# Kernel optimization log

Measured on AMD Instinct MI355X. Metric: run time of the kernel, lower is better.

Reference implementation:

```python
import jax, jax.numpy as jnp
import numpy as np

N_NODES = 100000
N_EDGES = 1600000
D = 128


def setup_inputs() -> dict:
    key = jax.random.key(0)
    ks = jax.random.split(key, 10)
    features = jax.random.normal(ks[0], (N_NODES, D), dtype=jnp.float32)
    edge_index = jax.random.randint(ks[1], (2, N_EDGES), 0, N_NODES, dtype=jnp.int64)
    edge_weight = jax.random.uniform(ks[2], (N_EDGES,), dtype=jnp.float32)
    scale = 1.0 / np.sqrt(D)
    W1 = jax.random.normal(ks[3], (D, D), dtype=jnp.float32) * scale
    b1 = jnp.zeros((D,), dtype=jnp.float32)
    a1 = jnp.full((D,), 0.25, dtype=jnp.float32)  # PReLU init
    W2 = jax.random.normal(ks[4], (D, D), dtype=jnp.float32) * scale
    b2 = jnp.zeros((D,), dtype=jnp.float32)
    a2 = jnp.full((D,), 0.25, dtype=jnp.float32)
    return {"features": features, "edge_index": edge_index, "edge_weight": edge_weight,
            "W1": W1, "b1": b1, "a1": a1, "W2": W2, "b2": b2, "a2": a2}


def _gcn_norm(edge_index, edge_weight, n_nodes):
    # PyG GCNConv default: add self-loops (weight 1), symmetric normalization.
    src, dst = edge_index[0], edge_index[1]
    loop = jnp.arange(n_nodes, dtype=src.dtype)
    src = jnp.concatenate([src, loop])
    dst = jnp.concatenate([dst, loop])
    w = jnp.concatenate([edge_weight, jnp.ones((n_nodes,), edge_weight.dtype)])
    deg = jax.ops.segment_sum(w, dst, num_segments=n_nodes)  # in-degree (target)
    dis = jnp.where(deg > 0, jax.lax.rsqrt(deg), 0.0)
    norm = dis[src] * w * dis[dst]  # [E + N]
    return src, dst, norm


def _gcn_layer(x, W, b, src, dst, norm, n_nodes):
    h = x @ W                                 # [N, D] dense GEMM first (PyG order)
    msg = h[src] * norm[:, None]              # gather + scale, [E+N, D]
    out = jax.ops.segment_sum(msg, dst, num_segments=n_nodes)
    return out + b


def _prelu(x, a):
    return jnp.where(x >= 0, x, a * x)


def reference(features, edge_index, edge_weight, W1, b1, a1, W2, b2, a2):
    n = features.shape[0]
    src, dst, norm = _gcn_norm(edge_index, edge_weight, n)
    # dropout is identity in eval mode
    x = _prelu(_gcn_layer(features, W1, b1, src, dst, norm, n), a1)
    x = _prelu(_gcn_layer(x, W2, b2, src, dst, norm, n), a2)
    return x
```

## Files before the change

kernel.cpp:

```cpp
#include <hip/hip_runtime.h>
#include <cstdint>

#define NN 100000
#define NE 1600000
#define DD 128
#define NB 250
#define BSZ 400

typedef unsigned int uint;
typedef unsigned short ushort;

typedef __attribute__((ext_vector_type(8))) short short8;
typedef __attribute__((ext_vector_type(4))) float floatx4;

__device__ inline uint f2bf(float f) {
    uint u = __float_as_uint(f);
    return (u + 0x7fffu + ((u >> 16) & 1u)) >> 16;
}


__global__ __launch_bounds__(256) void zero_bc(uint* __restrict__ bc) {
    if (threadIdx.x < NB) bc[threadIdx.x] = 0u;
}

__global__ __launch_bounds__(256) void bucket_hist(const int* __restrict__ dst,
                                                   uint* __restrict__ bc) {
    __shared__ uint h[NB];
    int tid = threadIdx.x;
    if (tid < NB) h[tid] = 0u;
    __syncthreads();
    int e0 = blockIdx.x * 8192 + tid;
#pragma unroll
    for (int k = 0; k < 32; ++k) {
        int e = e0 + 256 * k;
        if (e < NE) atomicAdd(&h[(uint)dst[e] / BSZ], 1u);
    }
    __syncthreads();
    if (tid < NB && h[tid]) atomicAdd(&bc[tid], h[tid]);
}

__global__ __launch_bounds__(256) void bucket_prefix(const uint* __restrict__ bc,
                                                     uint* __restrict__ bbase,
                                                     uint* __restrict__ bcur) {
    int lane = threadIdx.x;
    if (lane < 64) {
        uint v[4], s = 0;
#pragma unroll
        for (int k = 0; k < 4; ++k) {
            int i = lane * 4 + k;
            v[k] = (i < NB) ? bc[i] : 0u;
            s += v[k];
        }
        uint inc = s;
#pragma unroll
        for (int d = 1; d < 64; d <<= 1) {
            uint t = __shfl_up(inc, (unsigned)d, 64);
            if (lane >= d) inc += t;
        }
        uint run = inc - s;
#pragma unroll
        for (int k = 0; k < 4; ++k) {
            int i = lane * 4 + k;
            if (i < NB) { bbase[i] = run; bcur[i] = run; run += v[k]; }
        }
        if (lane == 63) bbase[NB] = run;
    }
}

__global__ __launch_bounds__(256) void bucket_append(const int* __restrict__ src,
                                                     const int* __restrict__ dst,
                                                     const float* __restrict__ w,
                                                     uint* __restrict__ bcur,
                                                     int2* __restrict__ etmp) {
    __shared__ uint h[NB];
    __shared__ uint res[NB];
    int tid = threadIdx.x;
    if (tid < NB) h[tid] = 0u;
    __syncthreads();
    int e0 = blockIdx.x * 4096 + tid;
    uint rank[16], bkt[16];
#pragma unroll
    for (int k = 0; k < 16; ++k) {
        int e = e0 + 256 * k;
        if (e < NE) {
            uint b = (uint)dst[e] / BSZ;
            bkt[k] = b;
            rank[k] = atomicAdd(&h[b], 1u);
        } else bkt[k] = 0xffffffffu;
    }
    __syncthreads();
    if (tid < NB) res[tid] = h[tid] ? atomicAdd(&bcur[tid], h[tid]) : 0u;
    __syncthreads();
#pragma unroll
    for (int k = 0; k < 16; ++k) {
        if (bkt[k] != 0xffffffffu) {
            int e = e0 + 256 * k;
            uint dl = (uint)dst[e] - bkt[k] * BSZ;
            uint wq = (uint)(w[e] * 8388608.0f);
            if (wq > 8388607u) wq = 8388607u;
            etmp[res[bkt[k]] + rank[k]] = make_int2(src[e], (int)((dl << 23) | wq));
        }
    }
}

__global__ __launch_bounds__(256) void bucket_build(const int2* __restrict__ etmp,
                                                    const uint* __restrict__ bbase,
                                                    float* __restrict__ dis,
                                                    int* __restrict__ hist_g,
                                                    int* __restrict__ rowstart,
                                                    int2* __restrict__ edges) {
    __shared__ float wdeg[BSZ];
    __shared__ uint  cnt[BSZ];
    __shared__ uint  cur[BSZ];
    __shared__ float disl[BSZ];
    int tid = threadIdx.x;
    int b = blockIdx.x;
    int n0 = b * BSZ;
    for (int i = tid; i < BSZ; i += 256) { wdeg[i] = 0.f; cnt[i] = 0u; }
    __syncthreads();
    uint base = bbase[b], end = bbase[b + 1];
    for (uint i = base + tid; i < end; i += 256) {
        uint y = (uint)etmp[i].y;
        uint dl = y >> 23;
        float wv = (float)(y & 0x7fffffu) * (1.0f / 8388608.0f);
        atomicAdd(&wdeg[dl], wv);
        atomicAdd(&cnt[dl], 1u);
    }
    __syncthreads();
    if (tid < 64) {
        uint v[7], s = 0;
#pragma unroll
        for (int k = 0; k < 7; ++k) {
            int i = tid * 7 + k;
            v[k] = (i < BSZ) ? cnt[i] : 0u;
            s += v[k];
        }
        uint inc = s;
#pragma unroll
        for (int d = 1; d < 64; d <<= 1) {
            uint t = __shfl_up(inc, (unsigned)d, 64);
            if (tid >= d) inc += t;
        }
        uint run = inc - s;
#pragma unroll
        for (int k = 0; k < 7; ++k) {
            int i = tid * 7 + k;
            if (i < BSZ) { cur[i] = run; run += v[k]; }
        }
    }
    __syncthreads();
    for (int i = tid; i < BSZ; i += 256) {
        float ds = rsqrtf(1.0f + wdeg[i]);
        disl[i] = ds;
        dis[n0 + i] = ds;
        hist_g[n0 + i] = (int)cnt[i];
        rowstart[n0 + i] = (int)(base + cur[i]);
    }
    __syncthreads();
    for (uint i = base + tid; i < end; i += 256) {
        int2 e = etmp[i];
        uint y = (uint)e.y;
        uint dl = y >> 23;
        float wv = (float)(y & 0x7fffffu) * (1.0f / 8388608.0f);
        uint p = atomicAdd(&cur[dl], 1u);
        float nrm = wv * disl[dl];
        edges[base + p] = make_int2(e.x, __float_as_int(nrm));
    }
}

#define WTS 136
__global__ __launch_bounds__(256) void gemm_mfma(const float* __restrict__ X,
                                                 const float* __restrict__ W,
                                                 const float* __restrict__ dis,
                                                 ushort* __restrict__ HB, int nrows) {
    __shared__ ushort Wt[DD * WTS];
    int tid = threadIdx.x;
#pragma unroll
    for (int it = 0; it < 16; ++it) {
        int flat = (tid + it * 256) * 4;
        int k = flat >> 7, n = flat & 127;
        float4 wv = *(const float4*)&W[flat];
        Wt[(n + 0) * WTS + k] = (ushort)f2bf(wv.x);
        Wt[(n + 1) * WTS + k] = (ushort)f2bf(wv.y);
        Wt[(n + 2) * WTS + k] = (ushort)f2bf(wv.z);
        Wt[(n + 3) * WTS + k] = (ushort)f2bf(wv.w);
    }
    __syncthreads();

    int wave = tid >> 6, lane = tid & 63;
    int q = lane >> 4, l16 = lane & 15;
    int row0 = blockIdx.x * 64 + wave * 16;

    int arow = row0 + l16;
    if (arow >= nrows) arow = nrows - 1;
    const float* xr = X + (size_t)arow * DD + q * 8;
    short8 afr[4];
#pragma unroll
    for (int ks = 0; ks < 4; ++ks) {
        float4 f0 = *(const float4*)(xr + ks * 32);
        float4 f1 = *(const float4*)(xr + ks * 32 + 4);
        uint4 u;
        u.x = f2bf(f0.x) | (f2bf(f0.y) << 16);
        u.y = f2bf(f0.z) | (f2bf(f0.w) << 16);
        u.z = f2bf(f1.x) | (f2bf(f1.y) << 16);
        u.w = f2bf(f1.z) | (f2bf(f1.w) << 16);
        afr[ks] = __builtin_bit_cast(short8, u);
    }

    floatx4 acc[8];
#pragma unroll
    for (int ct = 0; ct < 8; ++ct) acc[ct] = (floatx4)(0.0f);

#pragma unroll
    for (int ct = 0; ct < 8; ++ct) {
        const ushort* wp = &Wt[(ct * 16 + l16) * WTS + q * 8];
#pragma unroll
        for (int ks = 0; ks < 4; ++ks) {
            short8 bfr = *(const short8*)(wp + ks * 32);
            acc[ct] = __builtin_amdgcn_mfma_f32_16x16x32_bf16(afr[ks], bfr, acc[ct], 0, 0, 0);
        }
    }

#pragma unroll
    for (int reg = 0; reg < 4; ++reg) {
        int r = row0 + q * 4 + reg;
        if (r < nrows) {
            float ds = dis[r];
            ushort* orow = HB + (size_t)r * DD + l16;
#pragma unroll
            for (int ct = 0; ct < 8; ++ct)
                orow[ct * 16] = (ushort)f2bf(acc[ct][reg] * ds);
        }
    }
}

__device__ inline float4 bf4(uint2 u) {
    float4 f;
    f.x = __uint_as_float(u.x << 16);
    f.y = __uint_as_float(u.x & 0xffff0000u);
    f.z = __uint_as_float(u.y << 16);
    f.w = __uint_as_float(u.y & 0xffff0000u);
    return f;
}

__global__ __launch_bounds__(256) void gather_finalize(const ushort* __restrict__ hb,
                                                       const int2* __restrict__ edges,
                                                       const int* __restrict__ rowstart,
                                                       const int* __restrict__ hist,
                                                       const float* __restrict__ dis,
                                                       const float* __restrict__ b,
                                                       const float* __restrict__ a,
                                                       float* __restrict__ xout) {
    int tid = threadIdx.x;
    int lane = tid & 31;
    int node = blockIdx.x * 8 + (tid >> 5);

    int start = rowstart[node];
    int cnt = hist[node];
    float ds = dis[node];

    const uint2* hrow = (const uint2*)(hb + (size_t)node * DD) + lane;
    float4 self = bf4(*hrow);
    float4 acc0, acc1;
    acc0.x = self.x * ds; acc0.y = self.y * ds;
    acc0.z = self.z * ds; acc0.w = self.w * ds;
    acc1 = make_float4(0.f, 0.f, 0.f, 0.f);

    int j = 0;
    for (; j + 4 <= cnt; j += 4) {
        int2 e0 = edges[start + j];
        int2 e1 = edges[start + j + 1];
        int2 e2 = edges[start + j + 2];
        int2 e3 = edges[start + j + 3];
        uint2 u0 = *((const uint2*)(hb + (size_t)e0.x * DD) + lane);
        uint2 u1 = *((const uint2*)(hb + (size_t)e1.x * DD) + lane);
        uint2 u2 = *((const uint2*)(hb + (size_t)e2.x * DD) + lane);
        uint2 u3 = *((const uint2*)(hb + (size_t)e3.x * DD) + lane);
        float n0 = __int_as_float(e0.y), n1 = __int_as_float(e1.y);
        float n2 = __int_as_float(e2.y), n3 = __int_as_float(e3.y);
        float4 v0 = bf4(u0), v1 = bf4(u1), v2 = bf4(u2), v3 = bf4(u3);
        acc0.x += v0.x * n0; acc0.y += v0.y * n0; acc0.z += v0.z * n0; acc0.w += v0.w * n0;
        acc1.x += v1.x * n1; acc1.y += v1.y * n1; acc1.z += v1.z * n1; acc1.w += v1.w * n1;
        acc0.x += v2.x * n2; acc0.y += v2.y * n2; acc0.z += v2.z * n2; acc0.w += v2.w * n2;
        acc1.x += v3.x * n3; acc1.y += v3.y * n3; acc1.z += v3.z * n3; acc1.w += v3.w * n3;
    }
    for (; j < cnt; ++j) {
        int2 e = edges[start + j];
        uint2 u = *((const uint2*)(hb + (size_t)e.x * DD) + lane);
        float n = __int_as_float(e.y);
        float4 v = bf4(u);
        acc0.x += v.x * n; acc0.y += v.y * n; acc0.z += v.z * n; acc0.w += v.w * n;
    }

    float4 bb = ((const float4*)b)[lane];
    float4 aa = ((const float4*)a)[lane];
    float4 r;
    r.x = acc0.x + acc1.x + bb.x;
    r.y = acc0.y + acc1.y + bb.y;
    r.z = acc0.z + acc1.z + bb.z;
    r.w = acc0.w + acc1.w + bb.w;
    r.x = r.x >= 0.f ? r.x : aa.x * r.x;
    r.y = r.y >= 0.f ? r.y : aa.y * r.y;
    r.z = r.z >= 0.f ? r.z : aa.z * r.z;
    r.w = r.w >= 0.f ? r.w : aa.w * r.w;
    ((float4*)xout)[(size_t)node * 32 + lane] = r;
}

extern "C" void kernel_launch(void* const* d_in, const int* in_sizes, int n_in,
                              void* d_out, int out_size, void* d_ws, size_t ws_size,
                              hipStream_t stream) {
    const float* feat = (const float*)d_in[0];
    const int*   ei   = (const int*)d_in[1];
    const float* ew   = (const float*)d_in[2];
    const float* W1   = (const float*)d_in[3];
    const float* b1   = (const float*)d_in[4];
    const float* a1   = (const float*)d_in[5];
    const float* W2   = (const float*)d_in[6];
    const float* b2   = (const float*)d_in[7];
    const float* a2   = (const float*)d_in[8];
    float* out = (float*)d_out;

    const int* srcp = ei;
    const int* dstp = ei + NE;

    char* wsb = (char*)d_ws;
    size_t off = 0;
    uint* bc     = (uint*)(wsb + off); off += 4096;
    uint* bbase  = (uint*)(wsb + off); off += 4096;
    uint* bcur   = (uint*)(wsb + off); off += 4096;
    float* dis   = (float*)(wsb + off); off += 4ull * NN;
    int* hist    = (int*)(wsb + off); off += 4ull * NN;
    int* rowstart= (int*)(wsb + off); off += 4ull * NN;
    int2* etmp   = (int2*)(wsb + off); off += 8ull * NE;
    int2* edges  = (int2*)(wsb + off); off += 8ull * NE;
    ushort* hb   = (ushort*)(wsb + off); off += 2ull * NN * DD;
    float* x1    = out;

    zero_bc<<<1, 256, 0, stream>>>(bc);
    bucket_hist<<<(NE + 8191) / 8192, 256, 0, stream>>>(dstp, bc);
    bucket_prefix<<<1, 256, 0, stream>>>(bc, bbase, bcur);
    bucket_append<<<(NE + 4095) / 4096, 256, 0, stream>>>(srcp, dstp, ew, bcur, etmp);
    bucket_build<<<NB, 256, 0, stream>>>(etmp, bbase, dis, hist, rowstart, edges);

    const int gemm_blocks = (NN + 63) / 64;
    const int gath_blocks = NN / 8;

    gemm_mfma<<<gemm_blocks, 256, 0, stream>>>(feat, W1, dis, hb, NN);
    gather_finalize<<<gath_blocks, 256, 0, stream>>>(hb, edges, rowstart, hist, dis, b1, a1, x1);
    gemm_mfma<<<gemm_blocks, 256, 0, stream>>>(x1, W2, dis, hb, NN);
    gather_finalize<<<gath_blocks, 256, 0, stream>>>(hb, edges, rowstart, hist, dis, b2, a2, out);
}
```

Before: 375.3 us.

## Store layer-1 output as bf16, grid-stride GEMM, wider gather unroll, packed degree atomics

Layer-1 gather now writes its activations in bf16 to a new workspace buffer, and the second GEMM reads them directly without converting from fp32. This halves that intermediate traffic at the cost of rounding the stored activations to bf16. The GEMM becomes a grid-stride loop over 64-row tiles with half as many blocks, so each block's W-to-LDS transpose serves two tiles. The gather unrolls 8 edges per iteration with four accumulators to keep more loads in flight. bucket_build also packs the edge count and fixed-point weight sum into a single 64-bit LDS atomic instead of two atomics.

```diff
diff --git a/kernel.cpp b/kernel.cpp
--- a/kernel.cpp
+++ b/kernel.cpp
@@ -9,6 +9,7 @@
 
 typedef unsigned int uint;
 typedef unsigned short ushort;
+typedef unsigned long long u64;
 
 typedef __attribute__((ext_vector_type(8))) short short8;
 typedef __attribute__((ext_vector_type(4))) float floatx4;
@@ -109,22 +110,19 @@
                                                     int* __restrict__ hist_g,
                                                     int* __restrict__ rowstart,
                                                     int2* __restrict__ edges) {
-    __shared__ float wdeg[BSZ];
-    __shared__ uint  cnt[BSZ];
+    __shared__ u64   wc[BSZ];
     __shared__ uint  cur[BSZ];
     __shared__ float disl[BSZ];
     int tid = threadIdx.x;
     int b = blockIdx.x;
     int n0 = b * BSZ;
-    for (int i = tid; i < BSZ; i += 256) { wdeg[i] = 0.f; cnt[i] = 0u; }
+    for (int i = tid; i < BSZ; i += 256) wc[i] = 0ull;
     __syncthreads();
     uint base = bbase[b], end = bbase[b + 1];
     for (uint i = base + tid; i < end; i += 256) {
         uint y = (uint)etmp[i].y;
         uint dl = y >> 23;
-        float wv = (float)(y & 0x7fffffu) * (1.0f / 8388608.0f);
-        atomicAdd(&wdeg[dl], wv);
-        atomicAdd(&cnt[dl], 1u);
+        atomicAdd(&wc[dl], ((u64)1 << 40) | (u64)(y & 0x7fffffu));
     }
     __syncthreads();
     if (tid < 64) {
@@ -132,7 +130,7 @@
 #pragma unroll
         for (int k = 0; k < 7; ++k) {
             int i = tid * 7 + k;
-            v[k] = (i < BSZ) ? cnt[i] : 0u;
+            v[k] = (i < BSZ) ? (uint)(wc[i] >> 40) : 0u;
             s += v[k];
         }
         uint inc = s;
@@ -150,10 +148,12 @@
     }
     __syncthreads();
     for (int i = tid; i < BSZ; i += 256) {
-        float ds = rsqrtf(1.0f + wdeg[i]);
+        u64 v = wc[i];
+        float wsum = (float)(v & 0xffffffffffull) * (1.0f / 8388608.0f);
+        float ds = rsqrtf(1.0f + wsum);
         disl[i] = ds;
         dis[n0 + i] = ds;
-        hist_g[n0 + i] = (int)cnt[i];
+        hist_g[n0 + i] = (int)(v >> 40);
         rowstart[n0 + i] = (int)(base + cur[i]);
     }
     __syncthreads();
@@ -169,10 +169,13 @@
 }
 
 #define WTS 136
-__global__ __launch_bounds__(256) void gemm_mfma(const float* __restrict__ X,
+#define NTILES ((NN + 63) / 64)
+
+template <bool AF32>
+__global__ __launch_bounds__(256) void gemm_mfma(const void* __restrict__ Xv,
                                                  const float* __restrict__ W,
                                                  const float* __restrict__ dis,
-                                                 ushort* __restrict__ HB, int nrows) {
+                                                 ushort* __restrict__ HB) {
     __shared__ ushort Wt[DD * WTS];
     int tid = threadIdx.x;
 #pragma unroll
@@ -189,47 +192,57 @@
 
     int wave = tid >> 6, lane = tid & 63;
     int q = lane >> 4, l16 = lane & 15;
-    int row0 = blockIdx.x * 64 + wave * 16;
-
-    int arow = row0 + l16;
-    if (arow >= nrows) arow = nrows - 1;
-    const float* xr = X + (size_t)arow * DD + q * 8;
-    short8 afr[4];
-#pragma unroll
-    for (int ks = 0; ks < 4; ++ks) {
-        float4 f0 = *(const float4*)(xr + ks * 32);
-        float4 f1 = *(const float4*)(xr + ks * 32 + 4);
-        uint4 u;
-        u.x = f2bf(f0.x) | (f2bf(f0.y) << 16);
-        u.y = f2bf(f0.z) | (f2bf(f0.w) << 16);
-        u.z = f2bf(f1.x) | (f2bf(f1.y) << 16);
-        u.w = f2bf(f1.z) | (f2bf(f1.w) << 16);
-        afr[ks] = __builtin_bit_cast(short8, u);
-    }
-
-    floatx4 acc[8];
-#pragma unroll
-    for (int ct = 0; ct < 8; ++ct) acc[ct] = (floatx4)(0.0f);
-
-#pragma unroll
-    for (int ct = 0; ct < 8; ++ct) {
-        const ushort* wp = &Wt[(ct * 16 + l16) * WTS + q * 8];
-#pragma unroll
-        for (int ks = 0; ks < 4; ++ks) {
-            short8 bfr = *(const short8*)(wp + ks * 32);
-            acc[ct] = __builtin_amdgcn_mfma_f32_16x16x32_bf16(afr[ks], bfr, acc[ct], 0, 0, 0);
-        }
-    }
-
-#pragma unroll
-    for (int reg = 0; reg < 4; ++reg) {
-        int r = row0 + q * 4 + reg;
-        if (r < nrows) {
-            float ds = dis[r];
-            ushort* orow = HB + (size_t)r * DD + l16;
-#pragma unroll
-            for (int ct = 0; ct < 8; ++ct)
-                orow[ct * 16] = (ushort)f2bf(acc[ct][reg] * ds);
+
+    for (int tile = blockIdx.x; tile < NTILES; tile += gridDim.x) {
+        int row0 = tile * 64 + wave * 16;
+
+        int arow = row0 + l16;
+        if (arow >= NN) arow = NN - 1;
+        short8 afr[4];
+        if (AF32) {
+            const float* xr = (const float*)Xv + (size_t)arow * DD + q * 8;
+#pragma unroll
+            for (int ks = 0; ks < 4; ++ks) {
+                float4 f0 = *(const float4*)(xr + ks * 32);
+                float4 f1 = *(const float4*)(xr + ks * 32 + 4);
+                uint4 u;
+                u.x = f2bf(f0.x) | (f2bf(f0.y) << 16);
+                u.y = f2bf(f0.z) | (f2bf(f0.w) << 16);
+                u.z = f2bf(f1.x) | (f2bf(f1.y) << 16);
+                u.w = f2bf(f1.z) | (f2bf(f1.w) << 16);
+                afr[ks] = __builtin_bit_cast(short8, u);
+            }
+        } else {
+            const ushort* xr = (const ushort*)Xv + (size_t)arow * DD + q * 8;
+#pragma unroll
+            for (int ks = 0; ks < 4; ++ks)
+                afr[ks] = *(const short8*)(xr + ks * 32);
+        }
+
+        floatx4 acc[8];
+#pragma unroll
+        for (int ct = 0; ct < 8; ++ct) acc[ct] = (floatx4)(0.0f);
+
+#pragma unroll
+        for (int ct = 0; ct < 8; ++ct) {
+            const ushort* wp = &Wt[(ct * 16 + l16) * WTS + q * 8];
+#pragma unroll
+            for (int ks = 0; ks < 4; ++ks) {
+                short8 bfr = *(const short8*)(wp + ks * 32);
+                acc[ct] = __builtin_amdgcn_mfma_f32_16x16x32_bf16(afr[ks], bfr, acc[ct], 0, 0, 0);
+            }
+        }
+
+#pragma unroll
+        for (int reg = 0; reg < 4; ++reg) {
+            int r = row0 + q * 4 + reg;
+            if (r < NN) {
+                float ds = dis[r];
+                ushort* orow = HB + (size_t)r * DD + l16;
+#pragma unroll
+                for (int ct = 0; ct < 8; ++ct)
+                    orow[ct * 16] = (ushort)f2bf(acc[ct][reg] * ds);
+            }
         }
     }
 }
@@ -243,6 +256,7 @@
     return f;
 }
 
+template <bool BF16OUT>
 __global__ __launch_bounds__(256) void gather_finalize(const ushort* __restrict__ hb,
                                                        const int2* __restrict__ edges,
                                                        const int* __restrict__ rowstart,
@@ -250,42 +264,55 @@
                                                        const float* __restrict__ dis,
                                                        const float* __restrict__ b,
                                                        const float* __restrict__ a,
-                                                       float* __restrict__ xout) {
+                                                       void* __restrict__ xout) {
     int tid = threadIdx.x;
     int lane = tid & 31;
     int node = blockIdx.x * 8 + (tid >> 5);
 
-    int start = rowstart[node];
+    const int2* ep = edges + rowstart[node];
     int cnt = hist[node];
     float ds = dis[node];
 
     const uint2* hrow = (const uint2*)(hb + (size_t)node * DD) + lane;
     float4 self = bf4(*hrow);
-    float4 acc0, acc1;
+    float4 acc0, acc1, acc2, acc3;
     acc0.x = self.x * ds; acc0.y = self.y * ds;
     acc0.z = self.z * ds; acc0.w = self.w * ds;
     acc1 = make_float4(0.f, 0.f, 0.f, 0.f);
+    acc2 = make_float4(0.f, 0.f, 0.f, 0.f);
+    acc3 = make_float4(0.f, 0.f, 0.f, 0.f);
 
     int j = 0;
-    for (; j + 4 <= cnt; j += 4) {
-        int2 e0 = edges[start + j];
-        int2 e1 = edges[start + j + 1];
-        int2 e2 = edges[start + j + 2];
-        int2 e3 = edges[start + j + 3];
+    for (; j + 8 <= cnt; j += 8) {
+        int2 e0 = ep[j];     int2 e1 = ep[j + 1];
+        int2 e2 = ep[j + 2]; int2 e3 = ep[j + 3];
+        int2 e4 = ep[j + 4]; int2 e5 = ep[j + 5];
+        int2 e6 = ep[j + 6]; int2 e7 = ep[j + 7];
         uint2 u0 = *((const uint2*)(hb + (size_t)e0.x * DD) + lane);
         uint2 u1 = *((const uint2*)(hb + (size_t)e1.x * DD) + lane);
         uint2 u2 = *((const uint2*)(hb + (size_t)e2.x * DD) + lane);
         uint2 u3 = *((const uint2*)(hb + (size_t)e3.x * DD) + lane);
+        uint2 u4 = *((const uint2*)(hb + (size_t)e4.x * DD) + lane);
+        uint2 u5 = *((const uint2*)(hb + (size_t)e5.x * DD) + lane);
+        uint2 u6 = *((const uint2*)(hb + (size_t)e6.x * DD) + lane);
+        uint2 u7 = *((const uint2*)(hb + (size_t)e7.x * DD) + lane);
         float n0 = __int_as_float(e0.y), n1 = __int_as_float(e1.y);
         float n2 = __int_as_float(e2.y), n3 = __int_as_float(e3.y);
+        float n4 = __int_as_float(e4.y), n5 = __int_as_float(e5.y);
+        float n6 = __int_as_float(e6.y), n7 = __int_as_float(e7.y);
         float4 v0 = bf4(u0), v1 = bf4(u1), v2 = bf4(u2), v3 = bf4(u3);
+        float4 v4 = bf4(u4), v5 = bf4(u5), v6 = bf4(u6), v7 = bf4(u7);
         acc0.x += v0.x * n0; acc0.y += v0.y * n0; acc0.z += v0.z * n0; acc0.w += v0.w * n0;
         acc1.x += v1.x * n1; acc1.y += v1.y * n1; acc1.z += v1.z * n1; acc1.w += v1.w * n1;
-        acc0.x += v2.x * n2; acc0.y += v2.y * n2; acc0.z += v2.z * n2; acc0.w += v2.w * n2;
-        acc1.x += v3.x * n3; acc1.y += v3.y * n3; acc1.z += v3.z * n3; acc1.w += v3.w * n3;
+        acc2.x += v2.x * n2; acc2.y += v2.y * n2; acc2.z += v2.z * n2; acc2.w += v2.w * n2;
+        acc3.x += v3.x * n3; acc3.y += v3.y * n3; acc3.z += v3.z * n3; acc3.w += v3.w * n3;
+        acc0.x += v4.x * n4; acc0.y += v4.y * n4; acc0.z += v4.z * n4; acc0.w += v4.w * n4;
+        acc1.x += v5.x * n5; acc1.y += v5.y * n5; acc1.z += v5.z * n5; acc1.w += v5.w * n5;
+        acc2.x += v6.x * n6; acc2.y += v6.y * n6; acc2.z += v6.z * n6; acc2.w += v6.w * n6;
+        acc3.x += v7.x * n7; acc3.y += v7.y * n7; acc3.z += v7.z * n7; acc3.w += v7.w * n7;
     }
     for (; j < cnt; ++j) {
-        int2 e = edges[start + j];
+        int2 e = ep[j];
         uint2 u = *((const uint2*)(hb + (size_t)e.x * DD) + lane);
         float n = __int_as_float(e.y);
         float4 v = bf4(u);
@@ -295,15 +322,22 @@
     float4 bb = ((const float4*)b)[lane];
     float4 aa = ((const float4*)a)[lane];
     float4 r;
-    r.x = acc0.x + acc1.x + bb.x;
-    r.y = acc0.y + acc1.y + bb.y;
-    r.z = acc0.z + acc1.z + bb.z;
-    r.w = acc0.w + acc1.w + bb.w;
+    r.x = acc0.x + acc1.x + acc2.x + acc3.x + bb.x;
+    r.y = acc0.y + acc1.y + acc2.y + acc3.y + bb.y;
+    r.z = acc0.z + acc1.z + acc2.z + acc3.z + bb.z;
+    r.w = acc0.w + acc1.w + acc2.w + acc3.w + bb.w;
     r.x = r.x >= 0.f ? r.x : aa.x * r.x;
     r.y = r.y >= 0.f ? r.y : aa.y * r.y;
     r.z = r.z >= 0.f ? r.z : aa.z * r.z;
     r.w = r.w >= 0.f ? r.w : aa.w * r.w;
-    ((float4*)xout)[(size_t)node * 32 + lane] = r;
+    if (BF16OUT) {
+        uint2 o;
+        o.x = f2bf(r.x) | (f2bf(r.y) << 16);
+        o.y = f2bf(r.z) | (f2bf(r.w) << 16);
+        ((uint2*)xout)[(size_t)node * 32 + lane] = o;
+    } else {
+        ((float4*)xout)[(size_t)node * 32 + lane] = r;
+    }
 }
 
 extern "C" void kernel_launch(void* const* d_in, const int* in_sizes, int n_in,
@@ -334,7 +368,7 @@
     int2* etmp   = (int2*)(wsb + off); off += 8ull * NE;
     int2* edges  = (int2*)(wsb + off); off += 8ull * NE;
     ushort* hb   = (ushort*)(wsb + off); off += 2ull * NN * DD;
-    float* x1    = out;
+    ushort* x1b  = (ushort*)(wsb + off); off += 2ull * NN * DD;
 
     zero_bc<<<1, 256, 0, stream>>>(bc);
     bucket_hist<<<(NE + 8191) / 8192, 256, 0, stream>>>(dstp, bc);
@@ -342,11 +376,11 @@
     bucket_append<<<(NE + 4095) / 4096, 256, 0, stream>>>(srcp, dstp, ew, bcur, etmp);
     bucket_build<<<NB, 256, 0, stream>>>(etmp, bbase, dis, hist, rowstart, edges);
 
-    const int gemm_blocks = (NN + 63) / 64;
+    const int gemm_blocks = (NTILES + 1) / 2;
     const int gath_blocks = NN / 8;
 
-    gemm_mfma<<<gemm_blocks, 256, 0, stream>>>(feat, W1, dis, hb, NN);
-    gather_finalize<<<gath_blocks, 256, 0, stream>>>(hb, edges, rowstart, hist, dis, b1, a1, x1);
-    gemm_mfma<<<gemm_blocks, 256, 0, stream>>>(x1, W2, dis, hb, NN);
-    gather_finalize<<<gath_blocks, 256, 0, stream>>>(hb, edges, rowstart, hist, dis, b2, a2, out);
-}
+    gemm_mfma<true><<<gemm_blocks, 256, 0, stream>>>(feat, W1, dis, hb);
+    gather_finalize<true><<<gath_blocks, 256, 0, stream>>>(hb, edges, rowstart, hist, dis, b1, a1, x1b);
+    gemm_mfma<false><<<gemm_blocks, 256, 0, stream>>>(x1b, W2, dis, hb);
+    gather_finalize<false><<<gath_blocks, 256, 0, stream>>>(hb, edges, rowstart, hist, dis, b2, a2, out);
+}
```

Result: no change. 374.3 us (-0.3%).
